# Optimization experiments

Hardware: AMD Instinct MI355X
Metric: run time of the kernel (lower is better)

The kernel has to match this reference:

```python
import jax, jax.numpy as jnp
import numpy as np

N_EMBD = 1024
N_HEAD = 16

def _lin_params(key, fan_in, fan_out):
    kw, kb = jax.random.split(key)
    bound = 1.0 / np.sqrt(fan_in)
    W = jax.random.uniform(kw, (fan_in, fan_out), minval=-bound, maxval=bound, dtype=jnp.float32)
    b = jax.random.uniform(kb, (fan_out,), minval=-bound, maxval=bound, dtype=jnp.float32)
    return W, b

def setup_inputs() -> dict:
    key = jax.random.key(0)
    ks = jax.random.split(key, 6)
    x = jax.random.normal(ks[0], (2, 2048, N_EMBD), dtype=jnp.float32)
    W_attn, b_attn = _lin_params(ks[1], N_EMBD, 3 * N_EMBD)
    W_proj, b_proj = _lin_params(ks[2], N_EMBD, N_EMBD)
    W_fc, b_fc = _lin_params(ks[3], N_EMBD, 4 * N_EMBD)
    W_fc2, b_fc2 = _lin_params(ks[4], 4 * N_EMBD, N_EMBD)
    ln1_g = jnp.ones((N_EMBD,), jnp.float32); ln1_b = jnp.zeros((N_EMBD,), jnp.float32)
    ln2_g = jnp.ones((N_EMBD,), jnp.float32); ln2_b = jnp.zeros((N_EMBD,), jnp.float32)
    return {"x": x, "W_attn": W_attn, "b_attn": b_attn, "W_proj": W_proj, "b_proj": b_proj,
            "W_fc": W_fc, "b_fc": b_fc, "W_fc2": W_fc2, "b_fc2": b_fc2,
            "ln1_g": ln1_g, "ln1_b": ln1_b, "ln2_g": ln2_g, "ln2_b": ln2_b}

def _layernorm(x, g, b, eps=1e-5):
    mu = jnp.mean(x, axis=-1, keepdims=True)
    var = jnp.var(x, axis=-1, keepdims=True)
    return (x - mu) * jax.lax.rsqrt(var + eps) * g + b

def _attention(x, W_attn, b_attn, W_proj, b_proj):
    B, T, C = x.shape
    hd = C // N_HEAD
    qkv = x @ W_attn + b_attn                      # [B,T,3C]
    q, k, v = jnp.split(qkv, 3, axis=-1)
    # [B,T,C] -> [B,H,T,hd]
    q = q.reshape(B, T, N_HEAD, hd).transpose(0, 2, 1, 3)
    k = k.reshape(B, T, N_HEAD, hd).transpose(0, 2, 1, 3)
    v = v.reshape(B, T, N_HEAD, hd).transpose(0, 2, 1, 3)
    att = jnp.einsum('bhqd,bhkd->bhqk', q, k) * (1.0 / np.sqrt(hd))
    causal = jnp.tril(jnp.ones((T, T), bool))
    att = jnp.where(causal[None, None], att, -jnp.inf)
    att = jax.nn.softmax(att, axis=-1)
    y = jnp.einsum('bhqk,bhkd->bhqd', att, v)      # [B,H,T,hd]
    y = y.transpose(0, 2, 1, 3).reshape(B, T, C)
    return y @ W_proj + b_proj

def _mlp(x, W_fc, b_fc, W_fc2, b_fc2):
    h = jax.nn.gelu(x @ W_fc + b_fc, approximate=False)
    return h @ W_fc2 + b_fc2

def reference(x, W_attn, b_attn, W_proj, b_proj, W_fc, b_fc, W_fc2, b_fc2,
              ln1_g, ln1_b, ln2_g, ln2_b):
    x = x + _attention(_layernorm(x, ln1_g, ln1_b), W_attn, b_attn, W_proj, b_proj)
    x = x + _mlp(_layernorm(x, ln2_g, ln2_b), W_fc, b_fc, W_fc2, b_fc2)
    return x
```

## Files before the change

kernel.cpp:

```cpp
#include <hip/hip_runtime.h>
#include <cstdint>
#include <cstddef>


typedef unsigned short u16;
typedef short bf16x8 __attribute__((ext_vector_type(8)));
typedef float f32x4 __attribute__((ext_vector_type(4)));

#define C_EMBD 1024
#define T_SEQ  2048
#define N_BATCH 2
#define N_HEADS 16
#define HEAD_D 64
#define M_TOK  4096
#define Q_SCALE 0.18033688011112042f

__device__ __forceinline__ u16 f2b(float f) {
  union { float f; unsigned u; } v; v.f = f;
  unsigned r = (v.u + 0x7fffu + ((v.u >> 16) & 1u)) >> 16;
  return (u16)r;
}
__device__ __forceinline__ float b2f(u16 u) {
  union { unsigned u; float f; } v; v.u = ((unsigned)u) << 16;
  return v.f;
}
__device__ __forceinline__ unsigned pk2(float a, float b) {
  union { float f; unsigned u; } x, y; x.f = a; y.f = b;
  return __builtin_amdgcn_perm(y.u, x.u, 0x07060302u);
}
__device__ __forceinline__ void load_lds16(const void* g, void* l) {
  __builtin_amdgcn_global_load_lds(
      (const __attribute__((address_space(1))) void*)g,
      (__attribute__((address_space(3))) void*)l, 16, 0, 0);
}
__device__ __forceinline__ float gelu_fast(float x) {
  const float p = x * __builtin_fmaf(0.044715f * x, x, 1.0f);
  const float t = __builtin_amdgcn_exp2f(2.3021859215f * p);
  return x * t * __builtin_amdgcn_rcpf(t + 1.0f);
}

__global__ __launch_bounds__(256) void transpose_cast_all(
    const float* __restrict__ W0, u16* __restrict__ D0,
    const float* __restrict__ W1, u16* __restrict__ D1,
    const float* __restrict__ W2, u16* __restrict__ D2,
    const float* __restrict__ W3, u16* __restrict__ D3) {
  int id = blockIdx.x;
  const float* W; u16* D; int K, N, t;
  if (id < 3072)      { W = W0; D = D0; K = 1024; N = 3072; t = id; }
  else if (id < 4096) { W = W1; D = D1; K = 1024; N = 1024; t = id - 3072; }
  else if (id < 8192) { W = W2; D = D2; K = 1024; N = 4096; t = id - 4096; }
  else                { W = W3; D = D3; K = 4096; N = 1024; t = id - 8192; }
  const int nTN = N >> 5;
  const int n0 = (t % nTN) * 32, k0 = (t / nTN) * 32;
  __shared__ float tile[32][33];
  const int tx = threadIdx.x & 31, ty = threadIdx.x >> 5;
#pragma unroll
  for (int i = 0; i < 32; i += 8)
    tile[ty + i][tx] = W[(size_t)(k0 + ty + i) * N + n0 + tx];
  __syncthreads();
#pragma unroll
  for (int i = 0; i < 32; i += 8)
    D[(size_t)(n0 + ty + i) * K + k0 + tx] = f2b(tile[tx][ty + i]);
}

__global__ __launch_bounds__(256) void ln_cast(
    const float* __restrict__ X, const float* __restrict__ g,
    const float* __restrict__ b, u16* __restrict__ Y) {
  const int row = blockIdx.x;
  const int tid = threadIdx.x;
  const float4 v = ((const float4*)(X + (size_t)row * C_EMBD))[tid];
  float s = v.x + v.y + v.z + v.w;
  float ss = v.x * v.x + v.y * v.y + v.z * v.z + v.w * v.w;
#pragma unroll
  for (int off = 32; off > 0; off >>= 1) {
    s += __shfl_down(s, off, 64);
    ss += __shfl_down(ss, off, 64);
  }
  __shared__ float red[8];
  __shared__ float stats[2];
  const int wave = tid >> 6, lane = tid & 63;
  if (lane == 0) { red[wave] = s; red[4 + wave] = ss; }
  __syncthreads();
  if (tid == 0) {
    float S = red[0] + red[1] + red[2] + red[3];
    float SS = red[4] + red[5] + red[6] + red[7];
    float mu = S * (1.0f / C_EMBD);
    float var = SS * (1.0f / C_EMBD) - mu * mu;
    stats[0] = mu;
    stats[1] = rsqrtf(var + 1e-5f);
  }
  __syncthreads();
  const float mu = stats[0], rs = stats[1];
  const float4 gv = ((const float4*)g)[tid];
  const float4 bv = ((const float4*)b)[tid];
  ushort4 o;
  o.x = f2b((v.x - mu) * rs * gv.x + bv.x);
  o.y = f2b((v.y - mu) * rs * gv.y + bv.y);
  o.z = f2b((v.z - mu) * rs * gv.z + bv.z);
  o.w = f2b((v.w - mu) * rs * gv.w + bv.w);
  ((ushort4*)(Y + (size_t)row * C_EMBD))[tid] = o;
}

__global__ __launch_bounds__(256) void ln_reduce_cast(
    const float* __restrict__ P0, const float* __restrict__ P1,
    const float* __restrict__ bias, const float* __restrict__ res,
    const float* __restrict__ g, const float* __restrict__ b,
    float* __restrict__ X1, u16* __restrict__ Y) {
  const int row = blockIdx.x;
  const int tid = threadIdx.x;
  const size_t base = (size_t)row * C_EMBD;
  const float4 p0 = ((const float4*)(P0 + base))[tid];
  const float4 p1 = ((const float4*)(P1 + base))[tid];
  const float4 rr = ((const float4*)(res + base))[tid];
  const float4 bb = ((const float4*)bias)[tid];
  float4 v;
  v.x = p0.x + p1.x + rr.x + bb.x;
  v.y = p0.y + p1.y + rr.y + bb.y;
  v.z = p0.z + p1.z + rr.z + bb.z;
  v.w = p0.w + p1.w + rr.w + bb.w;
  ((float4*)(X1 + base))[tid] = v;
  float s = v.x + v.y + v.z + v.w;
  float ss = v.x * v.x + v.y * v.y + v.z * v.z + v.w * v.w;
#pragma unroll
  for (int off = 32; off > 0; off >>= 1) {
    s += __shfl_down(s, off, 64);
    ss += __shfl_down(ss, off, 64);
  }
  __shared__ float red[8];
  __shared__ float stats[2];
  const int wave = tid >> 6, lane = tid & 63;
  if (lane == 0) { red[wave] = s; red[4 + wave] = ss; }
  __syncthreads();
  if (tid == 0) {
    float S = red[0] + red[1] + red[2] + red[3];
    float SS = red[4] + red[5] + red[6] + red[7];
    float mu = S * (1.0f / C_EMBD);
    float var = SS * (1.0f / C_EMBD) - mu * mu;
    stats[0] = mu;
    stats[1] = rsqrtf(var + 1e-5f);
  }
  __syncthreads();
  const float mu = stats[0], rs = stats[1];
  const float4 gv = ((const float4*)g)[tid];
  const float4 bv = ((const float4*)b)[tid];
  ushort4 o;
  o.x = f2b((v.x - mu) * rs * gv.x + bv.x);
  o.y = f2b((v.y - mu) * rs * gv.y + bv.y);
  o.z = f2b((v.z - mu) * rs * gv.z + bv.z);
  o.w = f2b((v.w - mu) * rs * gv.w + bv.w);
  ((ushort4*)(Y + base))[tid] = o;
}

enum { EPI_BF16 = 0, EPI_GELU_BF16 = 2, EPI_PART = 3, EPI_QKV = 4 };

template <int EPI, int SPLIT>
__global__ __launch_bounds__(256) void gemm_bt(
    const u16* __restrict__ A, const u16* __restrict__ Bt,
    const float* __restrict__ bias,
    void* __restrict__ Cout, void* __restrict__ Cout2, void* __restrict__ Cout3,
    int M, int N, int K) {
  __shared__ u16 As[128 * 64];
  __shared__ u16 Bs[128 * 64];
  const int tid = threadIdx.x;
  const int wave = tid >> 6, lane = tid & 63;
  const int quad = lane >> 4, l16 = lane & 15;
  const int sw = l16 & 7;

  const int id = (int)blockIdx.y * (int)gridDim.x + (int)blockIdx.x;
  const int mt = ((id & 7) << 2) + ((id >> 3) & 3);
  const int nt_ = id >> 5;
  const int m0 = mt * 128, n0 = nt_ * 128;

  const int wm = (wave >> 1) * 64, wn = (wave & 1) * 64;

  f32x4 acc[4][4] = {};

  size_t aOff[4], bOff[4];
  int ldsOff[4];
#pragma unroll
  for (int i = 0; i < 4; ++i) {
    const int c = tid + i * 256;
    const int row = c >> 3, gc = ((c & 7) ^ (row & 7)) * 8;
    aOff[i] = (size_t)(m0 + row) * K + gc;
    bOff[i] = (size_t)(n0 + row) * K + gc;
    ldsOff[i] = c * 8;
  }

  const int kTiles = (K >> 6) / SPLIT;
  const int kt0 = (SPLIT == 2) ? (int)blockIdx.z * kTiles : 0;
  for (int kt = kt0; kt < kt0 + kTiles; ++kt) {
    const int k0 = kt << 6;
#pragma unroll
    for (int i = 0; i < 4; ++i)
      load_lds16(A + aOff[i] + k0, &As[ldsOff[i]]);
#pragma unroll
    for (int i = 0; i < 4; ++i)
      load_lds16(Bt + bOff[i] + k0, &Bs[ldsOff[i]]);
    __syncthreads();
#pragma unroll
    for (int ks = 0; ks < 2; ++ks) {
      bf16x8 aF[4], bF[4];
#pragma unroll
      for (int t = 0; t < 4; ++t) {
        aF[t] = *(const bf16x8*)
            &As[(wm + t * 16 + l16) * 64 + (((ks * 4 + quad) ^ sw) * 8)];
        bF[t] = *(const bf16x8*)
            &Bs[(wn + t * 16 + l16) * 64 + (((ks * 4 + quad) ^ sw) * 8)];
      }
#pragma unroll
      for (int tm = 0; tm < 4; ++tm)
#pragma unroll
        for (int tn = 0; tn < 4; ++tn)
          acc[tm][tn] = __builtin_amdgcn_mfma_f32_16x16x32_bf16(
              bF[tn], aF[tm], acc[tm][tn], 0, 0, 0);
    }
    __syncthreads();
  }

  float* Pz = (float*)((SPLIT == 2 && blockIdx.z == 1) ? Cout2 : Cout);
#pragma unroll
  for (int tm = 0; tm < 4; ++tm) {
    const int row = m0 + wm + tm * 16 + l16;
#pragma unroll
    for (int tn = 0; tn < 4; ++tn) {
      const int col = n0 + wn + tn * 16 + quad * 4;
      if constexpr (EPI == EPI_PART) {
        *(float4*)&Pz[(size_t)row * N + col] = *(float4*)&acc[tm][tn];
      } else {
        const float4 bz = *(const float4*)&bias[col];
        float v0 = acc[tm][tn][0] + bz.x, v1 = acc[tm][tn][1] + bz.y;
        float v2 = acc[tm][tn][2] + bz.z, v3 = acc[tm][tn][3] + bz.w;
        if constexpr (EPI == EPI_GELU_BF16) {
          v0 = gelu_fast(v0); v1 = gelu_fast(v1);
          v2 = gelu_fast(v2); v3 = gelu_fast(v3);
        }
        ushort4 o;
        o.x = f2b(v0); o.y = f2b(v1); o.z = f2b(v2); o.w = f2b(v3);
        *(ushort4*)&((u16*)Cout)[(size_t)row * N + col] = o;
      }
    }
  }
}

#define G_LOADA(MQ, PAR)                                                      \
  { const u16* Ab_ = &lds[(unsigned)((((MQ)*2 + (PAR))) << 13)];              \
    _Pragma("unroll") for (int t_ = 0; t_ < 4; ++t_)                          \
      _Pragma("unroll") for (int ks = 0; ks < 2; ++ks)                        \
        aF[t_][ks] = *(const bf16x8*)&Ab_[(wm * 64 + t_ * 16 + l16) * 64 +    \
                                          (((ks * 4 + quad) ^ sw) << 3)]; }
#define G_LOADB(BV, NQ, PAR)                                                  \
  { const u16* Bb_ = &lds[(unsigned)(((2 + (NQ)) * 2 + (PAR)) << 13)];        \
    _Pragma("unroll") for (int u_ = 0; u_ < 2; ++u_)                          \
      _Pragma("unroll") for (int ks = 0; ks < 2; ++ks)                        \
        BV[u_][ks] = *(const bf16x8*)&Bb_[(wn * 32 + u_ * 16 + l16) * 64 +    \
                                          (((ks * 4 + quad) ^ sw) << 3)]; }
#define G_MMA(MQ, NQ, BV)                                                     \
    _Pragma("unroll") for (int t_ = 0; t_ < 4; ++t_)                          \
      _Pragma("unroll") for (int u_ = 0; u_ < 2; ++u_)                        \
        _Pragma("unroll") for (int ks = 0; ks < 2; ++ks)                      \
          acc[(MQ)*4 + t_][(NQ)*2 + u_] =                                     \
              __builtin_amdgcn_mfma_f32_16x16x32_bf16(                        \
                  BV[u_][ks], aF[t_][ks], acc[(MQ)*4 + t_][(NQ)*2 + u_],      \
                  0, 0, 0);
#define G_BAR()   __builtin_amdgcn_s_barrier()
#define G_LGKM0() asm volatile("s_waitcnt lgkmcnt(0)" ::: "memory")
#define G_PRIO(x) __builtin_amdgcn_s_setprio(x)

template <int EPI, int SPLIT>
__global__ __launch_bounds__(512, 2) void gemm256(
    const u16* __restrict__ A, const u16* __restrict__ Bt,
    const float* __restrict__ bias,
    void* __restrict__ Cout, void* __restrict__ Cout2,
    void* __restrict__ Cout3, void* __restrict__ Cout4,
    int M, int N, int K) {
  __shared__ u16 lds[8 * 8192];
  const int tid = threadIdx.x;
  const int lane = tid & 63;
  const int wave = tid >> 6;
  const int quad = lane >> 4, l16 = lane & 15;
  const int sw = l16 & 7;
  const int wm = wave >> 2, wn = wave & 3;

  const int nTM = M >> 8, nTN = N >> 8;
  const int xcd = (int)blockIdx.x & 7;
  const int s = (int)blockIdx.x >> 3;
  const int gn = (nTN >= 6) ? 2 : 1;
  const int gm = 8 / gn;
  const int am = nTM / gm, bn = nTN / gn;
  const int bi = s / am;
  int ai = s % am;
  if (bi & 1) ai = am - 1 - ai;
  const int mt = (xcd % gm) * am + ai;
  const int ntl = (xcd / gm) * bn + bi;
  const int m0 = mt << 8, n0 = ntl << 8;

  f32x4 acc[8][4] = {};

  size_t aOffs[2][2], bOffs[2][2];
  int ldsc[2];
#pragma unroll
  for (int i = 0; i < 2; ++i) {
    const int c = tid + i * 512;
    const int r = c >> 3;
    const int scc = ((c & 7) ^ (r & 7)) << 3;
    ldsc[i] = c * 8;
    const int ra = ((r >> 6) << 7) + (r & 63);
    const int rb = ((r >> 5) << 6) + (r & 31);
    aOffs[0][i] = (size_t)(m0 + ra) * K + scc;
    aOffs[1][i] = (size_t)(m0 + ra + 64) * K + scc;
    bOffs[0][i] = (size_t)(n0 + rb) * K + scc;
    bOffs[1][i] = (size_t)(n0 + rb + 32) * K + scc;
  }
  auto stA = [&](int mq, int p, int kt) {
    u16* dst = &lds[(size_t)((mq * 2 + p) << 13)];
    const int k0 = kt << 6;
#pragma unroll
    for (int i = 0; i < 2; ++i)
      load_lds16(A + aOffs[mq][i] + k0, dst + ldsc[i]);
  };
  auto stB = [&](int nq, int p, int kt) {
    u16* dst = &lds[(size_t)(((2 + nq) * 2 + p) << 13)];
    const int k0 = kt << 6;
#pragma unroll
    for (int i = 0; i < 2; ++i)
      load_lds16(Bt + bOffs[nq][i] + k0, dst + ldsc[i]);
  };

  const int NT = (K >> 6) / SPLIT;
  const int kt0 = (SPLIT > 1) ? (int)blockIdx.z * NT : 0;

  stA(0, 0, kt0); stB(0, 0, kt0); stA(1, 0, kt0); stB(1, 0, kt0);
  stB(0, 1, kt0 + 1); stA(0, 1, kt0 + 1);
  asm volatile("s_waitcnt vmcnt(4)" ::: "memory");
  G_BAR();

  bf16x8 aF[4][2];
  bf16x8 bF0[2][2], bF1[2][2];

  for (int t = 0; t < NT; t += 2) {
#pragma unroll
    for (int p = 0; p < 2; ++p) {
      const int par = p;
      const int k1 = kt0 + (t + 1 + p < NT ? t + 1 + p : 0);
      const int k2 = kt0 + (t + 2 + p < NT ? t + 2 + p : 0);
      G_LOADA(0, par); G_LOADB(bF0, 0, par);
      stA(1, par ^ 1, k1);
      G_BAR(); G_LGKM0(); G_PRIO(1); G_MMA(0, 0, bF0); G_PRIO(0); G_BAR();
      G_LOADB(bF1, 1, par);
      stB(1, par ^ 1, k1);
      G_BAR(); G_LGKM0(); G_PRIO(1); G_MMA(0, 1, bF1); G_PRIO(0); G_BAR();
      G_LOADA(1, par);
      stA(0, par, k2);
      G_BAR(); G_LGKM0(); G_PRIO(1); G_MMA(1, 0, bF0); G_PRIO(0); G_BAR();
      stB(0, par, k2);
      G_BAR(); G_PRIO(1); G_MMA(1, 1, bF1); G_PRIO(0);
      asm volatile("s_waitcnt vmcnt(4)" ::: "memory");
      G_BAR();
    }
  }
  asm volatile("s_waitcnt vmcnt(0)" ::: "memory");

  if constexpr (EPI == EPI_PART) {
    const int z = (SPLIT > 1) ? (int)blockIdx.z : 0;
    float* Pz = (float*)(z == 0 ? Cout : z == 1 ? Cout2
                                       : z == 2 ? Cout3 : Cout4);
#pragma unroll
    for (int tm = 0; tm < 8; ++tm) {
      const int row = m0 + wm * 128 + tm * 16 + l16;
#pragma unroll
      for (int tn = 0; tn < 4; ++tn) {
        const int col = n0 + wn * 64 + tn * 16 + quad * 4;
        *(float4*)&Pz[(size_t)row * N + col] = *(float4*)&acc[tm][tn];
      }
    }
  } else if constexpr (EPI == EPI_QKV) {
#pragma unroll
    for (int tm = 0; tm < 8; ++tm) {
      const int row = m0 + wm * 128 + tm * 16 + l16;
      const int bb = row >> 11, tt = row & (T_SEQ - 1);
#pragma unroll
      for (int tn = 0; tn < 4; ++tn) {
        const int col = n0 + wn * 64 + tn * 16 + quad * 4;
        const float4 bz = *(const float4*)&bias[col];
        float v0 = acc[tm][tn][0] + bz.x, v1 = acc[tm][tn][1] + bz.y;
        float v2 = acc[tm][tn][2] + bz.z, v3 = acc[tm][tn][3] + bz.w;
        const int sec = col >> 10;
        const int h = (col & 1023) >> 6, d4 = col & 63;
        const int bh = bb * N_HEADS + h;
        if (sec == 0) {
          ushort4 o;
          o.x = f2b(v0 * Q_SCALE); o.y = f2b(v1 * Q_SCALE);
          o.z = f2b(v2 * Q_SCALE); o.w = f2b(v3 * Q_SCALE);
          *(ushort4*)&((u16*)Cout)[((size_t)bh * T_SEQ + tt) * HEAD_D + d4] = o;
        } else if (sec == 1) {
          ushort4 o;
          o.x = f2b(v0); o.y = f2b(v1); o.z = f2b(v2); o.w = f2b(v3);
          *(ushort4*)&((u16*)Cout2)[((size_t)bh * T_SEQ + tt) * HEAD_D + d4] = o;
        } else {
          u16* vp = (u16*)Cout3 + ((size_t)bh * HEAD_D + d4) * T_SEQ + tt;
          vp[0] = f2b(v0); vp[T_SEQ] = f2b(v1);
          vp[2 * T_SEQ] = f2b(v2); vp[3 * T_SEQ] = f2b(v3);
        }
      }
    }
  } else {
#pragma unroll
    for (int tm = 0; tm < 8; ++tm) {
      const int row = m0 + wm * 128 + tm * 16 + l16;
#pragma unroll
      for (int tn = 0; tn < 4; ++tn) {
        const int col = n0 + wn * 64 + tn * 16 + quad * 4;
        const float4 bz = *(const float4*)&bias[col];
        float v0 = acc[tm][tn][0] + bz.x, v1 = acc[tm][tn][1] + bz.y;
        float v2 = acc[tm][tn][2] + bz.z, v3 = acc[tm][tn][3] + bz.w;
        if constexpr (EPI == EPI_GELU_BF16) {
          v0 = gelu_fast(v0); v1 = gelu_fast(v1);
          v2 = gelu_fast(v2); v3 = gelu_fast(v3);
        }
        ushort4 o;
        o.x = f2b(v0); o.y = f2b(v1); o.z = f2b(v2); o.w = f2b(v3);
        *(ushort4*)&((u16*)Cout)[(size_t)row * N + col] = o;
      }
    }
  }
}

__global__ __launch_bounds__(256) void reduce_add4(
    const float* __restrict__ P0, const float* __restrict__ P1,
    const float* __restrict__ P2, const float* __restrict__ P3,
    const float* __restrict__ bias, const float* __restrict__ res,
    float* __restrict__ out) {
  const int idx = blockIdx.x * 256 + threadIdx.x;
  const float4 a = ((const float4*)P0)[idx];
  const float4 b = ((const float4*)P1)[idx];
  const float4 c = ((const float4*)P2)[idx];
  const float4 d = ((const float4*)P3)[idx];
  const float4 r = ((const float4*)res)[idx];
  const float4 g = ((const float4*)bias)[idx & 255];
  float4 o;
  o.x = a.x + b.x + c.x + d.x + r.x + g.x;
  o.y = a.y + b.y + c.y + d.y + r.y + g.y;
  o.z = a.z + b.z + c.z + d.z + r.z + g.z;
  o.w = a.w + b.w + c.w + d.w + r.w + g.w;
  ((float4*)out)[idx] = o;
}

__global__ __launch_bounds__(256, 4) void attn_fwd(
    const u16* __restrict__ Q, const u16* __restrict__ Kb,
    const u16* __restrict__ Vt, u16* __restrict__ Y) {
  const int id = (int)blockIdx.x;
  const int xcd = id & 7, slot = id >> 3;
  const int bh = xcd + ((slot & 3) << 3);
  const int qb = (T_SEQ / 64 - 1) - (slot >> 2);
  const int tid = threadIdx.x;
  const int wave = tid >> 6, lane = tid & 63;
  const int quad = lane >> 4, l16 = lane & 15;
  const int sw = l16 & 7;
  const u16* Qp = Q + (size_t)bh * T_SEQ * HEAD_D;
  const u16* Kp = Kb + (size_t)bh * T_SEQ * HEAD_D;
  const u16* Vp = Vt + (size_t)bh * HEAD_D * T_SEQ;

  __shared__ u16 Ks[2][64 * 64];
  __shared__ u16 Vs[2][64 * 64];
  __shared__ u16 Pl[4][16 * 64];

  const int c1 = tid, c2 = tid + 256;
  const int r1 = c1 >> 3, g1 = ((c1 & 7) ^ (r1 & 7)) * 8;
  const int r2 = c2 >> 3, g2 = ((c2 & 7) ^ (r2 & 7)) * 8;
  const size_t kO1 = (size_t)r1 * HEAD_D + g1, kO2 = (size_t)r2 * HEAD_D + g2;
  const size_t vO1 = (size_t)r1 * T_SEQ + g1, vO2 = (size_t)r2 * T_SEQ + g2;
  u16* const dK1[2] = {&Ks[0][c1 * 8], &Ks[1][c1 * 8]};
  u16* const dK2[2] = {&Ks[0][c2 * 8], &Ks[1][c2 * 8]};
  u16* const dV1[2] = {&Vs[0][c1 * 8], &Vs[1][c1 * 8]};
  u16* const dV2[2] = {&Vs[0][c2 * 8], &Vs[1][c2 * 8]};

  auto stageK = [&](int bb, int k0) {
    const u16* base = Kp + (size_t)k0 * HEAD_D;
    load_lds16(base + kO1, dK1[bb]);
    load_lds16(base + kO2, dK2[bb]);
  };
  auto stageV = [&](int bb, int k0) {
    const u16* base = Vp + k0;
    load_lds16(base + vO1, dV1[bb]);
    load_lds16(base + vO2, dV2[bb]);
  };

  const int b = bh >> 4, h = bh & 15;
  const int q0 = qb * 64;
  const int qglob = q0 + wave * 16 + l16;

  bf16x8 qF[2];
  qF[0] = *(const bf16x8*)&Qp[(size_t)qglob * HEAD_D + quad * 8];
  qF[1] = *(const bf16x8*)&Qp[(size_t)qglob * HEAD_D + 32 + quad * 8];

  f32x4 o[4] = {};
  float mrun = -3e38f, lrun = 0.0f;

  stageK(0, 0);
  stageV(0, 0);

  int buf = 0;
  for (int kb = 0; kb <= qb; ++kb) {
    const int k0 = kb * 64;
    __syncthreads();
    if (kb < qb) {
      stageK(buf ^ 1, k0 + 64);
      stageV(buf ^ 1, k0 + 64);
    }
    f32x4 st[4] = {};
#pragma unroll
    for (int ks = 0; ks < 2; ++ks) {
#pragma unroll
      for (int nt = 0; nt < 4; ++nt) {
        bf16x8 kF = *(const bf16x8*)
            &Ks[buf][(nt * 16 + l16) * 64 + (((ks * 4 + quad) ^ sw) * 8)];
        st[nt] = __builtin_amdgcn_mfma_f32_16x16x32_bf16(kF, qF[ks], st[nt],
                                                         0, 0, 0);
      }
    }
    if (kb == qb) {
#pragma unroll
      for (int nt = 0; nt < 4; ++nt) {
#pragma unroll
        for (int r = 0; r < 4; ++r) {
          const int key = k0 + nt * 16 + quad * 4 + r;
          if (key > qglob) st[nt][r] = -3e38f;
        }
      }
    }
    float m = st[0][0];
#pragma unroll
    for (int nt = 0; nt < 4; ++nt)
#pragma unroll
      for (int r = 0; r < 4; ++r) m = fmaxf(m, st[nt][r]);
    m = fmaxf(m, __shfl_xor(m, 16, 64));
    m = fmaxf(m, __shfl_xor(m, 32, 64));
    if (!__all(m - mrun <= 8.0f)) {
      const float nm = fmaxf(mrun, m);
      const float alpha = __builtin_amdgcn_exp2f(mrun - nm);
      mrun = nm;
      lrun *= alpha;
#pragma unroll
      for (int nt = 0; nt < 4; ++nt)
#pragma unroll
        for (int r = 0; r < 4; ++r) o[nt][r] *= alpha;
    }
    float sum = 0.0f;
#pragma unroll
    for (int nt = 0; nt < 4; ++nt)
#pragma unroll
      for (int r = 0; r < 4; ++r) {
        const float p = __builtin_amdgcn_exp2f(st[nt][r] - mrun);
        st[nt][r] = p;
        sum += p;
      }
    sum += __shfl_xor(sum, 16, 64);
    sum += __shfl_xor(sum, 32, 64);
    lrun += sum;
#pragma unroll
    for (int nt = 0; nt < 4; ++nt) {
      uint2 pk;
      pk.x = pk2(st[nt][0], st[nt][1]);
      pk.y = pk2(st[nt][2], st[nt][3]);
      const int wc = (((2 * nt + (quad >> 1)) ^ sw) << 3) + ((quad & 1) << 2);
      *(uint2*)&Pl[wave][(l16 << 6) + wc] = pk;
    }
#pragma unroll
    for (int ks = 0; ks < 2; ++ks) {
      bf16x8 aP = *(const bf16x8*)
          &Pl[wave][(l16 << 6) + (((ks * 4 + quad) ^ sw) << 3)];
#pragma unroll
      for (int nt = 0; nt < 4; ++nt) {
        bf16x8 vF = *(const bf16x8*)
            &Vs[buf][(nt * 16 + l16) * 64 + (((ks * 4 + quad) ^ sw) * 8)];
        o[nt] =
            __builtin_amdgcn_mfma_f32_16x16x32_bf16(vF, aP, o[nt], 0, 0, 0);
      }
    }
    buf ^= 1;
  }

  const float rl = 1.0f / lrun;
  u16* yp = Y + ((size_t)(b * T_SEQ + qglob)) * C_EMBD + h * HEAD_D;
#pragma unroll
  for (int nt = 0; nt < 4; ++nt) {
    ushort4 ov;
    ov.x = f2b(o[nt][0] * rl); ov.y = f2b(o[nt][1] * rl);
    ov.z = f2b(o[nt][2] * rl); ov.w = f2b(o[nt][3] * rl);
    *(ushort4*)&yp[nt * 16 + quad * 4] = ov;
  }
}

extern "C" void kernel_launch(void* const* d_in, const int* in_sizes, int n_in,
                              void* d_out, int out_size, void* d_ws,
                              size_t ws_size, hipStream_t stream) {
  const float* x      = (const float*)d_in[0];
  const float* W_attn = (const float*)d_in[1];
  const float* b_attn = (const float*)d_in[2];
  const float* W_proj = (const float*)d_in[3];
  const float* b_proj = (const float*)d_in[4];
  const float* W_fc   = (const float*)d_in[5];
  const float* b_fc   = (const float*)d_in[6];
  const float* W_fc2  = (const float*)d_in[7];
  const float* b_fc2  = (const float*)d_in[8];
  const float* ln1_g  = (const float*)d_in[9];
  const float* ln1_b  = (const float*)d_in[10];
  const float* ln2_g  = (const float*)d_in[11];
  const float* ln2_b  = (const float*)d_in[12];

  u16* wfc2T = (u16*)d_ws;
  float* x1  = (float*)(wfc2T + (size_t)1024 * 4096);
  u16* hbuf  = (u16*)(x1 + (size_t)M_TOK * C_EMBD);
  u16* dead  = hbuf + (size_t)M_TOK * 4096;
  u16* wqkvT = dead;
  u16* wprojT = wqkvT + (size_t)3072 * 1024;
  u16* wfcT  = wprojT + (size_t)1024 * 1024;
  u16* Abuf  = wfcT + (size_t)4096 * 1024;
  u16* Qb    = Abuf + (size_t)M_TOK * C_EMBD;
  u16* Kbuf  = Qb + (size_t)32 * T_SEQ * HEAD_D;
  u16* Vtb   = Kbuf + (size_t)32 * T_SEQ * HEAD_D;

  float* projP = (float*)hbuf;
  float* fc2P1 = (float*)dead;
  float* fc2P2 = fc2P1 + (size_t)M_TOK * C_EMBD;
  float* fc2P3 = fc2P2 + (size_t)M_TOK * C_EMBD;

  const dim3 blk(256);
  const dim3 blk512(512);

  transpose_cast_all<<<12288, blk, 0, stream>>>(
      W_attn, wqkvT, W_proj, wprojT, W_fc, wfcT, W_fc2, wfc2T);

  ln_cast<<<M_TOK, blk, 0, stream>>>(x, ln1_g, ln1_b, Abuf);

  gemm256<EPI_QKV, 1><<<dim3(192), blk512, 0, stream>>>(
      Abuf, wqkvT, b_attn, Qb, Kbuf, Vtb, nullptr, M_TOK, 3072, 1024);

  attn_fwd<<<dim3(1024), blk, 0, stream>>>(Qb, Kbuf, Vtb, Abuf);

  gemm_bt<EPI_PART, 2><<<dim3(1024 / 128, M_TOK / 128, 2), blk, 0, stream>>>(
      Abuf, wprojT, nullptr, projP, projP + (size_t)M_TOK * C_EMBD, nullptr,
      M_TOK, 1024, 1024);
  ln_reduce_cast<<<M_TOK, blk, 0, stream>>>(
      projP, projP + (size_t)M_TOK * C_EMBD, b_proj, x, ln2_g, ln2_b,
      x1, Abuf);

  gemm256<EPI_GELU_BF16, 1><<<dim3(256), blk512, 0, stream>>>(
      Abuf, wfcT, b_fc, hbuf, nullptr, nullptr, nullptr, M_TOK, 4096, 1024);

  gemm256<EPI_PART, 4><<<dim3(64, 1, 4), blk512, 0, stream>>>(
      hbuf, wfc2T, nullptr, d_out, fc2P1, fc2P2, fc2P3, M_TOK, 1024, 4096);
  reduce_add4<<<M_TOK * C_EMBD / 1024, blk, 0, stream>>>(
      (const float*)d_out, fc2P1, fc2P2, fc2P3, b_fc2, x1, (float*)d_out);
}
```

Baseline: 316.6 us.

## Simplify gemm256 pipeline to single-stage prefetch with full vmcnt drain per tile

```diff
diff --git a/kernel.cpp b/kernel.cpp
--- a/kernel.cpp
+++ b/kernel.cpp
@@ -242,18 +242,18 @@
   }
 }
 
-#define G_LOADA(MQ, PAR)                                                      \
+#define G_LOADA(DST, MQ, PAR)                                                 \
   { const u16* Ab_ = &lds[(unsigned)((((MQ)*2 + (PAR))) << 13)];              \
     _Pragma("unroll") for (int t_ = 0; t_ < 4; ++t_)                          \
       _Pragma("unroll") for (int ks = 0; ks < 2; ++ks)                        \
-        aF[t_][ks] = *(const bf16x8*)&Ab_[(wm * 64 + t_ * 16 + l16) * 64 +    \
-                                          (((ks * 4 + quad) ^ sw) << 3)]; }
-#define G_LOADB(BV, NQ, PAR)                                                  \
+        DST[t_][ks] = *(const bf16x8*)&Ab_[(wm * 64 + t_ * 16 + l16) * 64 +   \
+                                           (((ks * 4 + quad) ^ sw) << 3)]; }
+#define G_LOADB(DST, NQ, PAR)                                                 \
   { const u16* Bb_ = &lds[(unsigned)(((2 + (NQ)) * 2 + (PAR)) << 13)];        \
     _Pragma("unroll") for (int u_ = 0; u_ < 2; ++u_)                          \
       _Pragma("unroll") for (int ks = 0; ks < 2; ++ks)                        \
-        BV[u_][ks] = *(const bf16x8*)&Bb_[(wn * 32 + u_ * 16 + l16) * 64 +    \
-                                          (((ks * 4 + quad) ^ sw) << 3)]; }
+        DST[u_][ks] = *(const bf16x8*)&Bb_[(wn * 32 + u_ * 16 + l16) * 64 +   \
+                                           (((ks * 4 + quad) ^ sw) << 3)]; }
 #define G_MMA(MQ, NQ, BV)                                                     \
     _Pragma("unroll") for (int t_ = 0; t_ < 4; ++t_)                          \
       _Pragma("unroll") for (int u_ = 0; u_ < 2; ++u_)                        \
@@ -330,35 +330,27 @@
   const int kt0 = (SPLIT > 1) ? (int)blockIdx.z * NT : 0;
 
   stA(0, 0, kt0); stB(0, 0, kt0); stA(1, 0, kt0); stB(1, 0, kt0);
-  stB(0, 1, kt0 + 1); stA(0, 1, kt0 + 1);
-  asm volatile("s_waitcnt vmcnt(4)" ::: "memory");
+  asm volatile("s_waitcnt vmcnt(0)" ::: "memory");
   G_BAR();
 
   bf16x8 aF[4][2];
   bf16x8 bF0[2][2], bF1[2][2];
 
-  for (int t = 0; t < NT; t += 2) {
-#pragma unroll
-    for (int p = 0; p < 2; ++p) {
-      const int par = p;
-      const int k1 = kt0 + (t + 1 + p < NT ? t + 1 + p : 0);
-      const int k2 = kt0 + (t + 2 + p < NT ? t + 2 + p : 0);
-      G_LOADA(0, par); G_LOADB(bF0, 0, par);
-      stA(1, par ^ 1, k1);
-      G_BAR(); G_LGKM0(); G_PRIO(1); G_MMA(0, 0, bF0); G_PRIO(0); G_BAR();
-      G_LOADB(bF1, 1, par);
-      stB(1, par ^ 1, k1);
-      G_BAR(); G_LGKM0(); G_PRIO(1); G_MMA(0, 1, bF1); G_PRIO(0); G_BAR();
-      G_LOADA(1, par);
-      stA(0, par, k2);
-      G_BAR(); G_LGKM0(); G_PRIO(1); G_MMA(1, 0, bF0); G_PRIO(0); G_BAR();
-      stB(0, par, k2);
-      G_BAR(); G_PRIO(1); G_MMA(1, 1, bF1); G_PRIO(0);
-      asm volatile("s_waitcnt vmcnt(4)" ::: "memory");
-      G_BAR();
-    }
-  }
-  asm volatile("s_waitcnt vmcnt(0)" ::: "memory");
+  for (int t = 0; t < NT; ++t) {
+    const int par = t & 1;
+    const int k1 = kt0 + (t + 1 < NT ? t + 1 : 0);
+    G_LOADA(aF, 0, par); G_LOADB(bF0, 0, par); G_LOADB(bF1, 1, par);
+    stA(0, par ^ 1, k1); stB(0, par ^ 1, k1);
+    stA(1, par ^ 1, k1); stB(1, par ^ 1, k1);
+    G_BAR(); G_LGKM0();
+    G_PRIO(1); G_MMA(0, 0, bF0); G_MMA(0, 1, bF1); G_PRIO(0);
+    G_BAR();
+    G_LOADA(aF, 1, par);
+    G_BAR(); G_LGKM0();
+    G_PRIO(1); G_MMA(1, 0, bF0); G_MMA(1, 1, bF1); G_PRIO(0);
+    asm volatile("s_waitcnt vmcnt(0)" ::: "memory");
+    G_BAR();
+  }
 
   if constexpr (EPI == EPI_PART) {
     const int z = (SPLIT > 1) ? (int)blockIdx.z : 0;
```

Measured after the change: 336.0 us. +6.1%, slower.
